# Kernel tuning notes

Measured on AMD Instinct MI355X. Metric: run time of the kernel, lower is better.

Reference implementation:

```python
import jax, jax.numpy as jnp
import numpy as np

DECAY = 0.99
EPS = 1e-05
N_EMBED = 4096

def setup_inputs() -> dict:
    key = jax.random.key(0)
    k1, k2 = jax.random.split(key)
    x = jax.random.normal(k1, (32, 1024, 256), dtype=jnp.float32)
    embed = jax.random.normal(k2, (256, N_EMBED), dtype=jnp.float32)
    cluster_size = jnp.zeros((N_EMBED,), dtype=jnp.float32)
    embed_avg = embed  # buffer initialized as embed.clone()
    return {"x": x, "embed": embed, "cluster_size": cluster_size, "embed_avg": embed_avg}

def reference(x, embed, cluster_size, embed_avg):
    # x: [B, L, D]; embed/embed_avg: [D, K]; cluster_size: [K]
    B, L, D = x.shape
    K = embed.shape[1]
    flat = x.reshape(B * L, D)
    dist = (jnp.sum(flat * flat, axis=1, keepdims=True)
            - 2.0 * flat @ embed
            + jnp.sum(embed * embed, axis=0, keepdims=True))
    embed_indices = jnp.argmin(dist, axis=1)  # [N]
    # one-hot scatter-sum (counts per code)
    embed_onehot_sum = jnp.zeros((K,), dtype=x.dtype).at[embed_indices].add(1.0)
    # EMA updates, faithful to the torch source including its quirks:
    #   cluster_size.mul_(decay).add_(onehot_sum, alpha=1-eps)  (note: 1-eps, not 1-decay)
    #   embed_avg.mul_(decay).add(embed_sum, ...)  -> .add (not in-place), so embed_sum is discarded
    cluster_size_new = cluster_size * DECAY + embed_onehot_sum * (1.0 - EPS)
    embed_avg_new = embed_avg * DECAY
    n = jnp.sum(cluster_size_new)
    cs = (cluster_size_new + EPS) / (n + K * EPS) * n  # Laplace-smoothed counts
    embed_new = embed_avg_new / cs[None, :]  # [D, K], copied into self.embed before lookup
    # codebook lookup with the UPDATED embed (matches embed.data.copy_ ordering)
    quantize = embed_new.T[embed_indices].reshape(B, L, D)
    diff = jnp.mean(jnp.square(jax.lax.stop_gradient(quantize) - x))
    quantize_st = x + jax.lax.stop_gradient(quantize - x)  # straight-through
    return (quantize_st, embed_indices.reshape(B, L), diff,
            cluster_size_new, embed_avg_new, embed_new)
```

## Files before the change

### kernel.cpp

```cpp
#include <hip/hip_runtime.h>
#include <math.h>

constexpr float DECAY = 0.99f;
constexpr float EPS_F = 1e-5f;
constexpr float MARGIN = 0.08f;

typedef short bf16x8 __attribute__((ext_vector_type(8)));
typedef float f32x4 __attribute__((ext_vector_type(4)));

#define BM 128
#define BN 64
#define KSPLIT 4
#define D_FIX 256

__device__ __forceinline__ unsigned rne_bf16(float f) {
  unsigned u = __float_as_uint(f);
  return (u + 0x7fffu + ((u >> 16) & 1u)) >> 16;
}
__device__ __forceinline__ unsigned pack_hilo(float v) {
  unsigned u = __float_as_uint(v);
  unsigned hi = u & 0xffff0000u;
  float rem = v - __uint_as_float(hi);
  return hi | rne_bf16(rem);
}

__global__ void k_enorm(const float* __restrict__ e, double* __restrict__ e2d,
                        float* __restrict__ e2f, int D, int K) {
  __shared__ double red[4][64];
  const int kl = threadIdx.x & 63;
  const int part = threadIdx.x >> 6;
  const int k = blockIdx.x * 64 + kl;
  double s = 0.0;
  for (int d = part; d < D; d += 4) {
    double v = (double)e[(size_t)d * K + k];
    s = fma(v, v, s);
  }
  red[part][kl] = s;
  __syncthreads();
  if (part == 0) {
    double t = ((red[0][kl] + red[1][kl]) + red[2][kl]) + red[3][kl];
    e2d[k] = t;
    e2f[k] = (float)t;
  }
}

__launch_bounds__(256, 2)
__global__ void k_argmin_mfma(const float* __restrict__ x, const float* __restrict__ e,
                              const float* __restrict__ e2f,
                              float* __restrict__ bestv, float* __restrict__ secv,
                              int* __restrict__ besti, int N, int K) {
  __shared__ unsigned es[2][BN][32];
  __shared__ float e2s[1024];

  const int tid = threadIdx.x;
  const int w   = tid >> 6;
  const int l   = tid & 63;
  const int g   = l >> 4;
  const int c16 = l & 15;
  const int kslice = K / KSPLIT;
  const int kbase  = blockIdx.y * kslice;
  const int rowW   = blockIdx.x * BM + w * 32;

  for (int i = tid; i < 1024; i += 256) e2s[i] = e2f[kbase + i];

  bf16x8 xh[2][8], xl[2][8];
#pragma unroll
  for (int m = 0; m < 2; ++m) {
    const float* xr = x + (size_t)(rowW + m * 16 + c16) * D_FIX + 8 * g;
#pragma unroll
    for (int t = 0; t < 8; ++t) {
      float4 fa = *(const float4*)(xr + t * 32);
      float4 fb = *(const float4*)(xr + t * 32 + 4);
      float f[8] = {fa.x, fa.y, fa.z, fa.w, fb.x, fb.y, fb.z, fb.w};
      union { unsigned u[4]; bf16x8 v; } H, L;
#pragma unroll
      for (int p = 0; p < 4; ++p) {
        unsigned w0 = pack_hilo(f[2 * p]);
        unsigned w1 = pack_hilo(f[2 * p + 1]);
        H.u[p] = (w0 >> 16) | (w1 & 0xffff0000u);
        L.u[p] = (w0 & 0xffffu) | (w1 << 16);
      }
      xh[m][t] = H.v;
      xl[m][t] = L.v;
    }
  }

  float best[2][4], sec[2][4];
  int bidx[2][4];
#pragma unroll
  for (int m = 0; m < 2; ++m)
#pragma unroll
    for (int r = 0; r < 4; ++r) { best[m][r] = 3e38f; sec[m][r] = 3e38f; bidx[m][r] = 0; }

  float la[4][4];
  const int sq  = tid & 7;
  const int scq = 4 * ((tid >> 3) & 15);
  const bool stager = (tid < 128);

#define AM_LOAD(s_)                                                            \
  if (stager) {                                                                \
    const float* src = e + (size_t)(((s_) & 7) * 32 + sq * 4) * K              \
                         + (kbase + ((s_) >> 3) * 64 + scq);                   \
    _Pragma("unroll")                                                          \
    for (int i_ = 0; i_ < 4; ++i_) {                                           \
      float4 v_ = *(const float4*)(src + (size_t)i_ * K);                      \
      la[i_][0] = v_.x; la[i_][1] = v_.y; la[i_][2] = v_.z; la[i_][3] = v_.w;  \
    }                                                                          \
  }

#define AM_WRITE(buf_)                                                         \
  if (stager) {                                                                \
    _Pragma("unroll")                                                          \
    for (int j_ = 0; j_ < 4; ++j_) {                                           \
      int col_ = scq + j_;                                                     \
      uint4 pw_;                                                               \
      pw_.x = pack_hilo(la[0][j_]); pw_.y = pack_hilo(la[1][j_]);              \
      pw_.z = pack_hilo(la[2][j_]); pw_.w = pack_hilo(la[3][j_]);              \
      *(uint4*)&es[buf_][col_][(sq ^ (col_ & 7)) * 4] = pw_;                   \
    }                                                                          \
  }

  AM_LOAD(0);
  AM_WRITE(0);
  AM_LOAD(1);
  __syncthreads();

  int buf = 0;
  const int sw = c16 & 7;

  for (int kt = 0; kt < 16; ++kt) {
    f32x4 acc[2][4];
#pragma unroll
    for (int m = 0; m < 2; ++m)
#pragma unroll
      for (int c = 0; c < 4; ++c) acc[m][c] = (f32x4){0.f, 0.f, 0.f, 0.f};

#pragma unroll
    for (int t = 0; t < 8; ++t) {
#pragma unroll
      for (int c = 0; c < 4; ++c) {
        const int col = c * 16 + c16;
        const unsigned* ep = es[buf][col];
        uint4 q0 = *(const uint4*)&ep[((2 * g) ^ sw) * 4];
        uint4 q1 = *(const uint4*)&ep[((2 * g + 1) ^ sw) * 4];
        union { unsigned u[4]; bf16x8 v; } bh, bl;
        bh.u[0] = (q0.y & 0xffff0000u) | (q0.x >> 16);
        bl.u[0] = (q0.x & 0xffffu) | (q0.y << 16);
        bh.u[1] = (q0.w & 0xffff0000u) | (q0.z >> 16);
        bl.u[1] = (q0.z & 0xffffu) | (q0.w << 16);
        bh.u[2] = (q1.y & 0xffff0000u) | (q1.x >> 16);
        bl.u[2] = (q1.x & 0xffffu) | (q1.y << 16);
        bh.u[3] = (q1.w & 0xffff0000u) | (q1.z >> 16);
        bl.u[3] = (q1.z & 0xffffu) | (q1.w << 16);
#pragma unroll
        for (int m = 0; m < 2; ++m) {
          acc[m][c] = __builtin_amdgcn_mfma_f32_16x16x32_bf16(xh[m][t], bh.v, acc[m][c], 0, 0, 0);
          acc[m][c] = __builtin_amdgcn_mfma_f32_16x16x32_bf16(xh[m][t], bl.v, acc[m][c], 0, 0, 0);
          acc[m][c] = __builtin_amdgcn_mfma_f32_16x16x32_bf16(xl[m][t], bh.v, acc[m][c], 0, 0, 0);
        }
      }
      const int s = kt * 8 + t;
      if (s < 127) { AM_WRITE(buf ^ 1); }
      if (s < 126) { AM_LOAD(s + 2); }
      __syncthreads();
      buf ^= 1;
    }

#pragma unroll
    for (int c = 0; c < 4; ++c) {
      const int klocal = kt * 64 + c * 16 + c16;
      const float e2v = e2s[klocal];
      const int kg = kbase + klocal;
#pragma unroll
      for (int m = 0; m < 2; ++m)
#pragma unroll
        for (int r = 0; r < 4; ++r) {
          float dist = fmaf(-2.f, acc[m][c][r], e2v);
          if (dist < best[m][r]) { sec[m][r] = best[m][r]; best[m][r] = dist; bidx[m][r] = kg; }
          else sec[m][r] = fminf(sec[m][r], dist);
        }
    }
  }

#pragma unroll
  for (int off = 1; off < 16; off <<= 1) {
#pragma unroll
    for (int m = 0; m < 2; ++m)
#pragma unroll
      for (int r = 0; r < 4; ++r) {
        float ob = __shfl_xor(best[m][r], off);
        float os = __shfl_xor(sec[m][r], off);
        int   oi = __shfl_xor(bidx[m][r], off);
        if (ob < best[m][r] || (ob == best[m][r] && oi < bidx[m][r])) {
          sec[m][r] = fminf(best[m][r], os); best[m][r] = ob; bidx[m][r] = oi;
        } else {
          sec[m][r] = fminf(sec[m][r], ob);
        }
      }
  }

  if (c16 == 0) {
    const size_t base = (size_t)blockIdx.y * N;
#pragma unroll
    for (int m = 0; m < 2; ++m)
#pragma unroll
      for (int r = 0; r < 4; ++r) {
        int row = rowW + m * 16 + 4 * g + r;
        bestv[base + row] = best[m][r];
        secv[base + row]  = sec[m][r];
        besti[base + row] = bidx[m][r];
      }
  }
#undef AM_LOAD
#undef AM_WRITE
}

__global__ void k_combine(const float* __restrict__ bestv, const float* __restrict__ secv,
                          const int* __restrict__ besti, int* __restrict__ idx_out,
                          int* __restrict__ list, unsigned int* __restrict__ count, int N) {
  int n = blockIdx.x * blockDim.x + threadIdx.x;
  if (n >= N) return;
  float b = bestv[n], s = secv[n];
  int bi = besti[n];
#pragma unroll
  for (int p = 1; p < KSPLIT; ++p) {
    float ob = bestv[(size_t)p * N + n];
    float os = secv[(size_t)p * N + n];
    int   oi = besti[(size_t)p * N + n];
    if (ob < b || (ob == b && oi < bi)) { s = fminf(b, os); b = ob; bi = oi; }
    else s = fminf(s, ob);
  }
  idx_out[n] = bi;
  if (s - b < MARGIN) {
    unsigned int p = atomicAdd(count, 1u);
    list[p] = n;
  }
}

__launch_bounds__(256, 4)
__global__ void k_rescan(const float* __restrict__ x, const float* __restrict__ e,
                         const double* __restrict__ e2d, const int* __restrict__ list,
                         const unsigned int* __restrict__ count, int* __restrict__ idx_out,
                         int K) {
  __shared__ double xrow[D_FIX];
  __shared__ double rv[256];
  __shared__ int ri[256];
  const int tid = threadIdx.x;
  const unsigned int cnt = *count;
  for (unsigned int ii = blockIdx.x; ii < cnt; ii += gridDim.x) {
    const int row = list[ii];
    __syncthreads();
    xrow[tid] = (double)x[(size_t)row * D_FIX + tid];
    __syncthreads();
    double bb = 1e300; int bi = 0;
    for (int j = 0; j < K; j += 256) {
      const int k = j + tid;
      const float* ek = e + k;
      double a0 = 0.0, a1 = 0.0, a2 = 0.0, a3 = 0.0;
#pragma unroll 8
      for (int d = 0; d < D_FIX; d += 4) {
        a0 = fma(xrow[d + 0], (double)ek[(size_t)(d + 0) * K], a0);
        a1 = fma(xrow[d + 1], (double)ek[(size_t)(d + 1) * K], a1);
        a2 = fma(xrow[d + 2], (double)ek[(size_t)(d + 2) * K], a2);
        a3 = fma(xrow[d + 3], (double)ek[(size_t)(d + 3) * K], a3);
      }
      double dist = e2d[k] - 2.0 * ((a0 + a1) + (a2 + a3));
      if (dist < bb || (dist == bb && k < bi)) { bb = dist; bi = k; }
    }
    rv[tid] = bb; ri[tid] = bi;
    __syncthreads();
    for (int off = 128; off > 0; off >>= 1) {
      if (tid < off) {
        if (rv[tid + off] < rv[tid] || (rv[tid + off] == rv[tid] && ri[tid + off] < ri[tid])) {
          rv[tid] = rv[tid + off]; ri[tid] = ri[tid + off];
        }
      }
      __syncthreads();
    }
    if (tid == 0) idx_out[row] = ri[0];
    __syncthreads();
  }
}

__global__ void k_hist(const int* __restrict__ idx, unsigned int* __restrict__ cnt,
                       float* __restrict__ idxf_out, int N) {
  int n = blockIdx.x * blockDim.x + threadIdx.x;
  if (n >= N) return;
  int c = idx[n];
  idxf_out[n] = (float)c;
  atomicAdd(&cnt[c], 1u);
}

__global__ void k_cluster(const float* __restrict__ cs_in,
                          const unsigned int* __restrict__ cnt,
                          float* __restrict__ out_csn, float* __restrict__ cs_ws,
                          int K) {
  __shared__ double red[256];
  const int tid = threadIdx.x;
  double s = 0.0;
  for (int k = tid; k < K; k += 256) {
    float csn = cs_in[k] * DECAY + (float)cnt[k] * (1.0f - EPS_F);
    out_csn[k] = csn;
    s += (double)csn;
  }
  red[tid] = s;
  __syncthreads();
  for (int off = 128; off > 0; off >>= 1) {
    if (tid < off) red[tid] += red[tid + off];
    __syncthreads();
  }
  const float n = (float)red[0];
  const float denom = n + (float)K * EPS_F;
  for (int k = tid; k < K; k += 256) {
    float csn = out_csn[k];
    cs_ws[k] = (csn + EPS_F) / denom * n;
  }
}

__global__ void k_embed(const float* __restrict__ avg_in, const float* __restrict__ cs_ws,
                        float* __restrict__ out_avg, float* __restrict__ out_emb, int K) {
  int k = blockIdx.x * blockDim.x + threadIdx.x;
  int d = blockIdx.y;
  if (k >= K) return;
  size_t i = (size_t)d * K + k;
  float a = avg_in[i] * DECAY;
  out_avg[i] = a;
  out_emb[i] = a / cs_ws[k];
}

__global__ void k_transpose(const float* __restrict__ src, float* __restrict__ dst,
                            int D, int K) {
  __shared__ float t[64][65];
  const int kb = blockIdx.x * 64;
  const int db = blockIdx.y * 64;
  const int c = threadIdx.x & 63;
  const int r0 = (threadIdx.x >> 6) * 16;
  for (int i = 0; i < 16; ++i)
    t[r0 + i][c] = src[(size_t)(db + r0 + i) * K + kb + c];
  __syncthreads();
  for (int i = 0; i < 16; ++i)
    dst[(size_t)(kb + r0 + i) * D + db + c] = t[c][r0 + i];
}

__global__ void k_gather(const float* __restrict__ x, const float* __restrict__ embT,
                         const int* __restrict__ idx, float* __restrict__ out_q,
                         float* __restrict__ partial) {
  __shared__ float red[256];
  const int tid = threadIdx.x;
  const int n0 = blockIdx.x * 64;
  float s = 0.f;
  for (int u = 0; u < 16; ++u) {
    int i = u * 256 + tid;
    int row = n0 + (i >> 6);
    int f4 = (i & 63) * 4;
    int code = idx[row];
    float4 q  = *(const float4*)&embT[(size_t)code * D_FIX + f4];
    float4 xv = *(const float4*)&x[(size_t)row * D_FIX + f4];
    float4 dv = {q.x - xv.x, q.y - xv.y, q.z - xv.z, q.w - xv.w};
    float4 val = {xv.x + dv.x, xv.y + dv.y, xv.z + dv.z, xv.w + dv.w};
    *(float4*)&out_q[(size_t)row * D_FIX + f4] = val;
    s += dv.x * dv.x + dv.y * dv.y + dv.z * dv.z + dv.w * dv.w;
  }
  red[tid] = s;
  __syncthreads();
  for (int off = 128; off > 0; off >>= 1) {
    if (tid < off) red[tid] += red[tid + off];
    __syncthreads();
  }
  if (tid == 0) partial[blockIdx.x] = red[0];
}

__global__ void k_diff(const float* __restrict__ partial, float* __restrict__ out_diff,
                       int NB, long long total) {
  __shared__ double red[256];
  const int tid = threadIdx.x;
  double s = 0.0;
  for (int i = tid; i < NB; i += 256) s += (double)partial[i];
  red[tid] = s;
  __syncthreads();
  for (int off = 128; off > 0; off >>= 1) {
    if (tid < off) red[tid] += red[tid + off];
    __syncthreads();
  }
  if (tid == 0) out_diff[0] = (float)(red[0] / (double)total);
}

extern "C" void kernel_launch(void* const* d_in, const int* in_sizes, int n_in,
                              void* d_out, int out_size, void* d_ws, size_t ws_size,
                              hipStream_t stream) {
  const float* x            = (const float*)d_in[0];
  const float* embed        = (const float*)d_in[1];
  const float* cluster_size = (const float*)d_in[2];
  const float* embed_avg    = (const float*)d_in[3];

  const int K = in_sizes[2];
  const int D = in_sizes[1] / K;
  const int N = in_sizes[0] / D;

  float* out      = (float*)d_out;
  float* out_q    = out;
  float* out_idx  = out_q + (size_t)N * D;
  float* out_diff = out_idx + N;
  float* out_csn  = out_diff + 1;
  float* out_avg  = out_csn + K;
  float* out_emb  = out_avg + (size_t)D * K;

  char* ws = (char*)d_ws;
  double*       e2d     = (double*)ws;               ws += (size_t)K * 8;
  float*        e2f     = (float*)ws;                ws += (size_t)K * 4;
  int*          idx     = (int*)ws;                  ws += (size_t)N * 4;
  unsigned int* cnt     = (unsigned int*)ws;         ws += (size_t)K * 4;
  float*        cs_ws   = (float*)ws;                ws += (size_t)K * 4;
  float*        partial = (float*)ws;                ws += (size_t)(N / 64) * 4;
  float*        bestv   = (float*)ws;                ws += (size_t)KSPLIT * N * 4;
  float*        secv    = (float*)ws;                ws += (size_t)KSPLIT * N * 4;
  int*          besti   = (int*)ws;                  ws += (size_t)KSPLIT * N * 4;
  int*          list    = (int*)ws;                  ws += (size_t)N * 4;
  unsigned int* count   = (unsigned int*)ws;         ws += 64;
  float*        embT    = (float*)ws;                ws += (size_t)K * D * 4;

  hipMemsetAsync(cnt, 0, (size_t)K * sizeof(unsigned int), stream);
  hipMemsetAsync(count, 0, sizeof(unsigned int), stream);

  k_enorm<<<dim3(K / 64), dim3(256), 0, stream>>>(embed, e2d, e2f, D, K);
  k_argmin_mfma<<<dim3(N / BM, KSPLIT), dim3(256), 0, stream>>>(x, embed, e2f, bestv, secv,
                                                                besti, N, K);
  k_combine<<<dim3((N + 255) / 256), dim3(256), 0, stream>>>(bestv, secv, besti, idx,
                                                             list, count, N);
  k_rescan<<<dim3(1024), dim3(256), 0, stream>>>(x, embed, e2d, list, count, idx, K);
  k_hist<<<dim3((N + 255) / 256), dim3(256), 0, stream>>>(idx, cnt, out_idx, N);
  k_cluster<<<dim3(1), dim3(256), 0, stream>>>(cluster_size, cnt, out_csn, cs_ws, K);
  k_embed<<<dim3((K + 255) / 256, D), dim3(256), 0, stream>>>(embed_avg, cs_ws, out_avg, out_emb, K);
  k_transpose<<<dim3(K / 64, D / 64), dim3(256), 0, stream>>>(out_emb, embT, D, K);
  k_gather<<<dim3(N / 64), dim3(256), 0, stream>>>(x, embT, idx, out_q, partial);
  k_diff<<<dim3(1), dim3(256), 0, stream>>>(partial, out_diff, N / 64, (long long)N * D);
}
```

Measured before the change: 454.5 us.

## Prepack codebook into swizzled bf16 hi/lo tiles and stream via global_load_lds

A new prepass kernel splits the codebook into bf16 hi/lo halves once, laid out in pre-swizzled 64x64 tiles. The argmin kernel then copies these tiles straight into LDS with direct global-to-LDS loads, double buffered. This removes the per-block float loads, packing and register unpacking from the inner loop. KSPLIT drops from 4 to 2, which gives fewer blocks and larger LDS tiles (32KB plus 8KB e2s), at the cost of an extra kernel launch and a workspace pass over the codebook.

```diff
diff --git a/kernel.cpp b/kernel.cpp
--- a/kernel.cpp
+++ b/kernel.cpp
@@ -9,8 +9,8 @@
 typedef float f32x4 __attribute__((ext_vector_type(4)));
 
 #define BM 128
-#define BN 64
-#define KSPLIT 4
+#define KSPLIT 2
+#define NU 128
 #define D_FIX 256
 
 __device__ __forceinline__ unsigned rne_bf16(float f) {
@@ -22,6 +22,28 @@
   unsigned hi = u & 0xffff0000u;
   float rem = v - __uint_as_float(hi);
   return hi | rne_bf16(rem);
+}
+
+__global__ void k_prepack(const float* __restrict__ e, ushort* __restrict__ phl, int K) {
+  __shared__ ushort tile[8192];
+  const int unit = blockIdx.x;
+  const int ct = unit >> 2, du = unit & 3;
+  const int t = threadIdx.x;
+#pragma unroll
+  for (int p = 0; p < 16; ++p) {
+    int idx = t + p * 256;
+    int dl = idx >> 6, col = idx & 63;
+    float v = e[(size_t)(du * 64 + dl) * K + ct * 64 + col];
+    unsigned pk = pack_hilo(v);
+    int pos = col * 64 + (((dl >> 3) ^ (col & 7)) << 3) + (dl & 7);
+    tile[pos] = (ushort)(pk >> 16);
+    tile[4096 + pos] = (ushort)(pk & 0xffffu);
+  }
+  __syncthreads();
+  uint4* dst = (uint4*)(phl + (size_t)unit * 8192);
+  const uint4* srcT = (const uint4*)tile;
+#pragma unroll
+  for (int p = 0; p < 4; ++p) dst[t + p * 256] = srcT[t + p * 256];
 }
 
 __global__ void k_enorm(const float* __restrict__ e, double* __restrict__ e2d,
@@ -45,23 +67,36 @@
 }
 
 __launch_bounds__(256, 2)
-__global__ void k_argmin_mfma(const float* __restrict__ x, const float* __restrict__ e,
+__global__ void k_argmin_mfma(const float* __restrict__ x, const ushort* __restrict__ phl,
                               const float* __restrict__ e2f,
                               float* __restrict__ bestv, float* __restrict__ secv,
                               int* __restrict__ besti, int N, int K) {
-  __shared__ unsigned es[2][BN][32];
-  __shared__ float e2s[1024];
+  __shared__ ushort es[2][8192];
+  __shared__ float e2s[2048];
 
   const int tid = threadIdx.x;
   const int w   = tid >> 6;
   const int l   = tid & 63;
   const int g   = l >> 4;
   const int c16 = l & 15;
-  const int kslice = K / KSPLIT;
-  const int kbase  = blockIdx.y * kslice;
-  const int rowW   = blockIdx.x * BM + w * 32;
-
-  for (int i = tid; i < 1024; i += 256) e2s[i] = e2f[kbase + i];
+  const int kbase = blockIdx.y * (K / KSPLIT);
+  const int rowW  = blockIdx.x * BM + w * 32;
+
+  char* esb = (char*)es;
+
+#define STAGE(u_, b_) do {                                                          \
+    const char* gs_ = (const char*)phl +                                            \
+        (((size_t)blockIdx.y * NU + (size_t)(u_)) << 14) + (w << 12) + (l << 4);    \
+    char* ld_ = esb + ((b_) << 14) + (w << 12);                                     \
+    __builtin_amdgcn_global_load_lds((const unsigned*)(gs_),        (unsigned*)(ld_),        16, 0, 0); \
+    __builtin_amdgcn_global_load_lds((const unsigned*)(gs_ + 1024), (unsigned*)(ld_ + 1024), 16, 0, 0); \
+    __builtin_amdgcn_global_load_lds((const unsigned*)(gs_ + 2048), (unsigned*)(ld_ + 2048), 16, 0, 0); \
+    __builtin_amdgcn_global_load_lds((const unsigned*)(gs_ + 3072), (unsigned*)(ld_ + 3072), 16, 0, 0); \
+  } while (0)
+
+  STAGE(0, 0);
+
+  for (int i = tid; i < 2048; i += 256) e2s[i] = e2f[kbase + i];
 
   bf16x8 xh[2][8], xl[2][8];
 #pragma unroll
@@ -92,95 +127,59 @@
 #pragma unroll
     for (int r = 0; r < 4; ++r) { best[m][r] = 3e38f; sec[m][r] = 3e38f; bidx[m][r] = 0; }
 
-  float la[4][4];
-  const int sq  = tid & 7;
-  const int scq = 4 * ((tid >> 3) & 15);
-  const bool stager = (tid < 128);
-
-#define AM_LOAD(s_)                                                            \
-  if (stager) {                                                                \
-    const float* src = e + (size_t)(((s_) & 7) * 32 + sq * 4) * K              \
-                         + (kbase + ((s_) >> 3) * 64 + scq);                   \
-    _Pragma("unroll")                                                          \
-    for (int i_ = 0; i_ < 4; ++i_) {                                           \
-      float4 v_ = *(const float4*)(src + (size_t)i_ * K);                      \
-      la[i_][0] = v_.x; la[i_][1] = v_.y; la[i_][2] = v_.z; la[i_][3] = v_.w;  \
-    }                                                                          \
-  }
-
-#define AM_WRITE(buf_)                                                         \
-  if (stager) {                                                                \
-    _Pragma("unroll")                                                          \
-    for (int j_ = 0; j_ < 4; ++j_) {                                           \
-      int col_ = scq + j_;                                                     \
-      uint4 pw_;                                                               \
-      pw_.x = pack_hilo(la[0][j_]); pw_.y = pack_hilo(la[1][j_]);              \
-      pw_.z = pack_hilo(la[2][j_]); pw_.w = pack_hilo(la[3][j_]);              \
-      *(uint4*)&es[buf_][col_][(sq ^ (col_ & 7)) * 4] = pw_;                   \
-    }                                                                          \
-  }
-
-  AM_LOAD(0);
-  AM_WRITE(0);
-  AM_LOAD(1);
-  __syncthreads();
-
-  int buf = 0;
-  const int sw = c16 & 7;
-
-  for (int kt = 0; kt < 16; ++kt) {
-    f32x4 acc[2][4];
-#pragma unroll
-    for (int m = 0; m < 2; ++m)
-#pragma unroll
-      for (int c = 0; c < 4; ++c) acc[m][c] = (f32x4){0.f, 0.f, 0.f, 0.f};
-
-#pragma unroll
-    for (int t = 0; t < 8; ++t) {
+  const int sw16 = ((g ^ (c16 & 7)) << 4);
+  const char* thr0 = esb + c16 * 128;
+
+  f32x4 acc[2][4];
+
+  for (int u = 0; u < NU; ++u) {
+    __syncthreads();
+    if (u + 1 < NU) STAGE(u + 1, (u + 1) & 1);
+    const int kt = u >> 2, du = u & 3;
+
+    if (du == 0) {
+#pragma unroll
+      for (int m = 0; m < 2; ++m)
+#pragma unroll
+        for (int c = 0; c < 4; ++c) acc[m][c] = (f32x4){0.f, 0.f, 0.f, 0.f};
+    }
+
+    const char* pbuf = thr0 + ((u & 1) << 14);
+#pragma unroll
+    for (int tt = 0; tt < 2; ++tt) {
+      const int t = 2 * du + tt;
+      const char* pt = pbuf + (sw16 ^ (tt << 6));
 #pragma unroll
       for (int c = 0; c < 4; ++c) {
-        const int col = c * 16 + c16;
-        const unsigned* ep = es[buf][col];
-        uint4 q0 = *(const uint4*)&ep[((2 * g) ^ sw) * 4];
-        uint4 q1 = *(const uint4*)&ep[((2 * g + 1) ^ sw) * 4];
-        union { unsigned u[4]; bf16x8 v; } bh, bl;
-        bh.u[0] = (q0.y & 0xffff0000u) | (q0.x >> 16);
-        bl.u[0] = (q0.x & 0xffffu) | (q0.y << 16);
-        bh.u[1] = (q0.w & 0xffff0000u) | (q0.z >> 16);
-        bl.u[1] = (q0.z & 0xffffu) | (q0.w << 16);
-        bh.u[2] = (q1.y & 0xffff0000u) | (q1.x >> 16);
-        bl.u[2] = (q1.x & 0xffffu) | (q1.y << 16);
-        bh.u[3] = (q1.w & 0xffff0000u) | (q1.z >> 16);
-        bl.u[3] = (q1.z & 0xffffu) | (q1.w << 16);
+        bf16x8 bh = *(const bf16x8*)(pt + c * 2048);
+        bf16x8 bl = *(const bf16x8*)(pt + c * 2048 + 8192);
 #pragma unroll
         for (int m = 0; m < 2; ++m) {
-          acc[m][c] = __builtin_amdgcn_mfma_f32_16x16x32_bf16(xh[m][t], bh.v, acc[m][c], 0, 0, 0);
-          acc[m][c] = __builtin_amdgcn_mfma_f32_16x16x32_bf16(xh[m][t], bl.v, acc[m][c], 0, 0, 0);
-          acc[m][c] = __builtin_amdgcn_mfma_f32_16x16x32_bf16(xl[m][t], bh.v, acc[m][c], 0, 0, 0);
+          acc[m][c] = __builtin_amdgcn_mfma_f32_16x16x32_bf16(xh[m][t], bh, acc[m][c], 0, 0, 0);
+          acc[m][c] = __builtin_amdgcn_mfma_f32_16x16x32_bf16(xh[m][t], bl, acc[m][c], 0, 0, 0);
+          acc[m][c] = __builtin_amdgcn_mfma_f32_16x16x32_bf16(xl[m][t], bh, acc[m][c], 0, 0, 0);
         }
       }
-      const int s = kt * 8 + t;
-      if (s < 127) { AM_WRITE(buf ^ 1); }
-      if (s < 126) { AM_LOAD(s + 2); }
-      __syncthreads();
-      buf ^= 1;
-    }
-
-#pragma unroll
-    for (int c = 0; c < 4; ++c) {
-      const int klocal = kt * 64 + c * 16 + c16;
-      const float e2v = e2s[klocal];
-      const int kg = kbase + klocal;
-#pragma unroll
-      for (int m = 0; m < 2; ++m)
-#pragma unroll
-        for (int r = 0; r < 4; ++r) {
-          float dist = fmaf(-2.f, acc[m][c][r], e2v);
-          if (dist < best[m][r]) { sec[m][r] = best[m][r]; best[m][r] = dist; bidx[m][r] = kg; }
-          else sec[m][r] = fminf(sec[m][r], dist);
-        }
-    }
-  }
+    }
+
+    if (du == 3) {
+#pragma unroll
+      for (int c = 0; c < 4; ++c) {
+        const int klocal = kt * 64 + c * 16 + c16;
+        const float e2v = e2s[klocal];
+        const int kg = kbase + klocal;
+#pragma unroll
+        for (int m = 0; m < 2; ++m)
+#pragma unroll
+          for (int r = 0; r < 4; ++r) {
+            float dist = fmaf(-2.f, acc[m][c][r], e2v);
+            if (dist < best[m][r]) { sec[m][r] = best[m][r]; best[m][r] = dist; bidx[m][r] = kg; }
+            else sec[m][r] = fminf(sec[m][r], dist);
+          }
+      }
+    }
+  }
+#undef STAGE
 
 #pragma unroll
   for (int off = 1; off < 16; off <<= 1) {
@@ -211,8 +210,6 @@
         besti[base + row] = bidx[m][r];
       }
   }
-#undef AM_LOAD
-#undef AM_WRITE
 }
 
 __global__ void k_combine(const float* __restrict__ bestv, const float* __restrict__ secv,
@@ -418,12 +415,14 @@
   int*          list    = (int*)ws;                  ws += (size_t)N * 4;
   unsigned int* count   = (unsigned int*)ws;         ws += 64;
   float*        embT    = (float*)ws;                ws += (size_t)K * D * 4;
+  ushort*       phl     = (ushort*)ws;               ws += (size_t)K * D * 4;
 
   hipMemsetAsync(cnt, 0, (size_t)K * sizeof(unsigned int), stream);
   hipMemsetAsync(count, 0, sizeof(unsigned int), stream);
 
+  k_prepack<<<dim3((K / 64) * 4), dim3(256), 0, stream>>>(embed, phl, K);
   k_enorm<<<dim3(K / 64), dim3(256), 0, stream>>>(embed, e2d, e2f, D, K);
-  k_argmin_mfma<<<dim3(N / BM, KSPLIT), dim3(256), 0, stream>>>(x, embed, e2f, bestv, secv,
+  k_argmin_mfma<<<dim3(N / BM, KSPLIT), dim3(256), 0, stream>>>(x, phl, e2f, bestv, secv,
                                                                 besti, N, K);
   k_combine<<<dim3((N + 255) / 256), dim3(256), 0, stream>>>(bestv, secv, besti, idx,
                                                              list, count, N);
```

After: 498.6 us. +9.7%, slower.
